# Performance work log

Measured on AMD Instinct MI355X. Metric: run time of the kernel, lower is better.

The kernel has to match this reference:

```python
import jax, jax.numpy as jnp
import numpy as np
from jax import lax

WINDOW = 11
C1 = (0.01 * 1) ** 2
C2 = (0.03 * 1) ** 2


def setup_inputs() -> dict:
    key = jax.random.key(0)
    kx, ky = jax.random.split(key)
    x = jax.random.uniform(kx, (8, 3, 512, 512), dtype=jnp.float32)
    y = jax.random.uniform(ky, (8, 3, 512, 512), dtype=jnp.float32)
    return {"x": x, "y": y}


def _window_sum(a):
    # sum over every overlapping WINDOW x WINDOW patch (stride 1, valid)
    return lax.reduce_window(a, 0.0, lax.add,
                             (1, 1, WINDOW, WINDOW),
                             (1, 1, 1, 1), 'VALID')


def reference(x, y):
    # x, y: [B, C, H, W] images in [0, 1]
    n = float(WINDOW * WINDOW)
    sx = _window_sum(x)
    sy = _window_sum(y)
    sxx = _window_sum(x * x)
    syy = _window_sum(y * y)
    sxy = _window_sum(x * y)
    mx = sx / n
    my = sy / n
    # unbiased variance / covariance (matches torch var(unbiased=True) and
    # the bessel-corrected covariance in the original)
    vx = (sxx - n * mx * mx) / (n - 1.0)
    vy = (syy - n * my * my) / (n - 1.0)
    cov = (sxy - n * mx * my) / (n - 1.0)
    ssim = (2.0 * mx * my + C1) * (2.0 * cov + C2) / (
        (mx * mx + my * my + C1) * (vx + vy + C2))
    # original averages over windows (dim 0) and channels (dim 2) -> per-batch
    return (1.0 - ssim.mean(axis=(1, 2, 3))) / 2.0
```

## Files before the change

kernel.cpp:

```cpp
#include <hip/hip_runtime.h>

#define WINDOW 11
#define H 512
#define W 512
#define OH 502
#define OW 502
#define NCH 3
#define BATCH 8
#define RSTRIPE 8
#define NSTRIPES 63
#define NGRP 5
#define GRPW 118
#define WAVES_PER_IMG (NSTRIPES * NGRP)
#define NWAVES (BATCH * NCH * WAVES_PER_IMG)
#define WAVES_PER_BATCH (NCH * WAVES_PER_IMG)
#define NXCD 8
#define CHUNK (NWAVES / NXCD)

#define NPIX_PER_BATCH (3.0f * 502.0f * 502.0f)

template <int CTRL, int RM>
__device__ __forceinline__ float scan_step(float x) {
    int s = __builtin_amdgcn_update_dpp(0, __builtin_bit_cast(int, x),
                                        CTRL, RM, 0xf, false);
    return x + __builtin_bit_cast(float, s);
}
__device__ __forceinline__ float wave_iscan(float x) {
    x = scan_step<0x111, 0xf>(x);
    x = scan_step<0x112, 0xf>(x);
    x = scan_step<0x114, 0xf>(x);
    x = scan_step<0x118, 0xf>(x);
    x = scan_step<0x142, 0xa>(x);
    x = scan_step<0x143, 0xc>(x);
    return x;
}

__device__ __forceinline__ float ssim_from(float sx, float sy, float s2, float sxy) {
    const float n = 121.0f;
    const float inv_n = 1.0f / 121.0f;
    const float inv_nm1 = 1.0f / 120.0f;
    const float c1 = 1e-4f;
    const float c2 = 9e-4f;
    float mx  = sx * inv_n;
    float my  = sy * inv_n;
    float mxy = mx * my;
    float m2  = mx * mx + my * my;
    float cov = (sxy - n * mxy) * inv_nm1;
    float v2  = (s2  - n * m2)  * inv_nm1;
    float num = (2.f * mxy + c1) * (2.f * cov + c2);
    float den = (m2 + c1) * (v2 + c2);
    return num * __builtin_amdgcn_rcpf(den);
}

__global__ __launch_bounds__(64) void ssim_main(const float* __restrict__ x,
                                                const float* __restrict__ y,
                                                float* __restrict__ partials) {
    const int lane = threadIdx.x & 63;

    const int wg    = blockIdx.x;
    const int w_lin = (wg % NXCD) * CHUNK + wg / NXCD;

    const int img = w_lin / WAVES_PER_IMG;
    const int rem = w_lin % WAVES_PER_IMG;
    const int grp = rem / NSTRIPES;
    const int rs  = rem % NSTRIPES;

    const int i0 = rs * RSTRIPE;
    const int i1 = min(i0 + RSTRIPE, OH);
    const int cstart = grp * GRPW;
    const int outw   = min(GRPW, OW - cstart);
    const int c0 = min(cstart + 2 * lane, W - 2);
    const bool tapActive = (2 * lane < outw);

    const float* __restrict__ xc = x + (size_t)img * H * W + c0;
    const float* __restrict__ yc = y + (size_t)img * H * W + c0;

    float4 v0 = make_float4(0.f, 0.f, 0.f, 0.f);
    float4 v1 = make_float4(0.f, 0.f, 0.f, 0.f);
#pragma unroll
    for (int r = 0; r < WINDOW; ++r) {
        float2 a = *(const float2*)(xc + (size_t)(i0 + r) * W);
        float2 b = *(const float2*)(yc + (size_t)(i0 + r) * W);
        v0.x += a.x; v0.y += b.x; v0.z += a.x * a.x + b.x * b.x; v0.w += a.x * b.x;
        v1.x += a.y; v1.y += b.y; v1.z += a.y * a.y + b.y * b.y; v1.w += a.y * b.y;
    }

#define LD(j, xo, yo, xn, yn) do {                                  \
        int jc_ = min((j), H - 1);                                   \
        int rn_ = min((j) + WINDOW, H - 1);                          \
        xo = *(const float2*)(xc + (size_t)jc_ * W);                 \
        yo = *(const float2*)(yc + (size_t)jc_ * W);                 \
        xn = *(const float2*)(xc + (size_t)rn_ * W);                 \
        yn = *(const float2*)(yc + (size_t)rn_ * W);                 \
    } while (0)

#define SLIDE(xo, yo, xn, yn) do {                                   \
        v0.x += xn.x - xo.x;                                          \
        v0.y += yn.x - yo.x;                                          \
        v0.z += xn.x * xn.x + yn.x * yn.x - xo.x * xo.x - yo.x * yo.x;\
        v0.w += xn.x * yn.x - xo.x * yo.x;                            \
        v1.x += xn.y - xo.y;                                          \
        v1.y += yn.y - yo.y;                                          \
        v1.z += xn.y * xn.y + yn.y * yn.y - xo.y * xo.y - yo.y * yo.y;\
        v1.w += xn.y * yn.y - xo.y * yo.y;                            \
    } while (0)

    float acc = 0.f;

#define COMPUTE() do {                                                        \
        float Tx = v0.x + v1.x, Ty = v0.y + v1.y;                             \
        float Tz = v0.z + v1.z, Tw = v0.w + v1.w;                             \
        float Sx = wave_iscan(Tx), Sy = wave_iscan(Ty);                       \
        float Sz = wave_iscan(Tz), Sw = wave_iscan(Tw);                       \
        int src = lane + 5;                                                   \
        float Ax = __shfl(Sx, src, 64), Ay = __shfl(Sy, src, 64);             \
        float Az = __shfl(Sz, src, 64), Aw = __shfl(Sw, src, 64);             \
        float Bx = __shfl(v1.x, src, 64), By = __shfl(v1.y, src, 64);         \
        float Bz = __shfl(v1.z, src, 64), Bw = __shfl(v1.w, src, 64);         \
        if (tapActive) {                                                      \
            acc += ssim_from(Ax - Bx - Sx + Tx, Ay - By - Sy + Ty,            \
                             Az - Bz - Sz + Tz, Aw - Bw - Sw + Tw);           \
            acc += ssim_from(Ax - Sx + v1.x, Ay - Sy + v1.y,                  \
                             Az - Sz + v1.z, Aw - Sw + v1.w);                 \
        }                                                                     \
    } while (0)

    float2 xoA, yoA, xnA, ynA, xoB, yoB, xnB, ynB;
    LD(i0,     xoA, yoA, xnA, ynA);
    LD(i0 + 1, xoB, yoB, xnB, ynB);
    for (int i = i0; i < i1; i += 2) {
        COMPUTE();
        SLIDE(xoA, yoA, xnA, ynA);
        LD(i + 2, xoA, yoA, xnA, ynA);
        COMPUTE();
        SLIDE(xoB, yoB, xnB, ynB);
        LD(i + 3, xoB, yoB, xnB, ynB);
    }

    for (int off = 32; off > 0; off >>= 1)
        acc += __shfl_down(acc, off, 64);
    if (lane == 0) partials[w_lin] = acc;
}

__global__ __launch_bounds__(256) void ssim_reduce(const float* __restrict__ partials,
                                                   float* __restrict__ out) {
    const int b = blockIdx.x;
    const int t = threadIdx.x;
    float s = 0.f;
    for (int k = t; k < WAVES_PER_BATCH; k += 256)
        s += partials[b * WAVES_PER_BATCH + k];
    for (int off = 32; off > 0; off >>= 1)
        s += __shfl_down(s, off, 64);
    __shared__ float red[4];
    int wid = t >> 6, lane = t & 63;
    if (lane == 0) red[wid] = s;
    __syncthreads();
    if (t == 0) {
        float tot = (red[0] + red[1]) + (red[2] + red[3]);
        out[b] = (1.0f - tot / NPIX_PER_BATCH) * 0.5f;
    }
}

extern "C" void kernel_launch(void* const* d_in, const int* in_sizes, int n_in,
                              void* d_out, int out_size, void* d_ws, size_t ws_size,
                              hipStream_t stream) {
    const float* x = (const float*)d_in[0];
    const float* y = (const float*)d_in[1];
    float* out      = (float*)d_out;
    float* partials = (float*)d_ws;

    ssim_main<<<NWAVES, 64, 0, stream>>>(x, y, partials);
    ssim_reduce<<<BATCH, 256, 0, stream>>>(partials, out);
}
```

Baseline: 28.29 us.

## Keep sliding-window rows in register ring and use taller row stripes

Stores the 11 rows of the current vertical window in a register ring buffer so each input row is loaded from memory once instead of twice (as new and as leaving row). Row stripes grow from 8 to 33 rows to amortize the 11-row prologue, with a mask for rows past the output edge. The reduce kernel drops its loop since partials per batch now fit one block. This trades fewer waves and higher register pressure for less memory traffic.

```diff
diff --git a/kernel.cpp b/kernel.cpp
--- a/kernel.cpp
+++ b/kernel.cpp
@@ -7,8 +7,8 @@
 #define OW 502
 #define NCH 3
 #define BATCH 8
-#define RSTRIPE 8
-#define NSTRIPES 63
+#define RSTRIPE 33
+#define NSTRIPES 16
 #define NGRP 5
 #define GRPW 118
 #define WAVES_PER_IMG (NSTRIPES * NGRP)
@@ -75,39 +75,42 @@
     const float* __restrict__ xc = x + (size_t)img * H * W + c0;
     const float* __restrict__ yc = y + (size_t)img * H * W + c0;
 
+    float2 fx[11], fy[11];
     float4 v0 = make_float4(0.f, 0.f, 0.f, 0.f);
     float4 v1 = make_float4(0.f, 0.f, 0.f, 0.f);
 #pragma unroll
     for (int r = 0; r < WINDOW; ++r) {
         float2 a = *(const float2*)(xc + (size_t)(i0 + r) * W);
         float2 b = *(const float2*)(yc + (size_t)(i0 + r) * W);
+        fx[r] = a; fy[r] = b;
         v0.x += a.x; v0.y += b.x; v0.z += a.x * a.x + b.x * b.x; v0.w += a.x * b.x;
         v1.x += a.y; v1.y += b.y; v1.z += a.y * a.y + b.y * b.y; v1.w += a.y * b.y;
     }
 
-#define LD(j, xo, yo, xn, yn) do {                                  \
+    float2 nx, ny;
+#define LDNEW(j) do {                                                \
         int jc_ = min((j), H - 1);                                   \
-        int rn_ = min((j) + WINDOW, H - 1);                          \
-        xo = *(const float2*)(xc + (size_t)jc_ * W);                 \
-        yo = *(const float2*)(yc + (size_t)jc_ * W);                 \
-        xn = *(const float2*)(xc + (size_t)rn_ * W);                 \
-        yn = *(const float2*)(yc + (size_t)rn_ * W);                 \
+        nx = *(const float2*)(xc + (size_t)jc_ * W);                 \
+        ny = *(const float2*)(yc + (size_t)jc_ * W);                 \
     } while (0)
 
-#define SLIDE(xo, yo, xn, yn) do {                                   \
-        v0.x += xn.x - xo.x;                                          \
-        v0.y += yn.x - yo.x;                                          \
-        v0.z += xn.x * xn.x + yn.x * yn.x - xo.x * xo.x - yo.x * yo.x;\
-        v0.w += xn.x * yn.x - xo.x * yo.x;                            \
-        v1.x += xn.y - xo.y;                                          \
-        v1.y += yn.y - yo.y;                                          \
-        v1.z += xn.y * xn.y + yn.y * yn.y - xo.y * xo.y - yo.y * yo.y;\
-        v1.w += xn.y * yn.y - xo.y * yo.y;                            \
+#define SLIDE(u) do {                                                 \
+        v0.x += nx.x - fx[u].x;                                       \
+        v0.y += ny.x - fy[u].x;                                       \
+        v0.z += nx.x * nx.x + ny.x * ny.x                             \
+              - fx[u].x * fx[u].x - fy[u].x * fy[u].x;                \
+        v0.w += nx.x * ny.x - fx[u].x * fy[u].x;                      \
+        v1.x += nx.y - fx[u].y;                                       \
+        v1.y += ny.y - fy[u].y;                                       \
+        v1.z += nx.y * nx.y + ny.y * ny.y                             \
+              - fx[u].y * fx[u].y - fy[u].y * fy[u].y;                \
+        v1.w += nx.y * ny.y - fx[u].y * fy[u].y;                      \
+        fx[u] = nx; fy[u] = ny;                                       \
     } while (0)
 
     float acc = 0.f;
 
-#define COMPUTE() do {                                                        \
+#define COMPUTE(rowActive) do {                                               \
         float Tx = v0.x + v1.x, Ty = v0.y + v1.y;                             \
         float Tz = v0.z + v1.z, Tw = v0.w + v1.w;                             \
         float Sx = wave_iscan(Tx), Sy = wave_iscan(Ty);                       \
@@ -117,7 +120,7 @@
         float Az = __shfl(Sz, src, 64), Aw = __shfl(Sw, src, 64);             \
         float Bx = __shfl(v1.x, src, 64), By = __shfl(v1.y, src, 64);         \
         float Bz = __shfl(v1.z, src, 64), Bw = __shfl(v1.w, src, 64);         \
-        if (tapActive) {                                                      \
+        if (tapActive & (rowActive)) {                                        \
             acc += ssim_from(Ax - Bx - Sx + Tx, Ay - By - Sy + Ty,            \
                              Az - Bz - Sz + Tz, Aw - Bw - Sw + Tw);           \
             acc += ssim_from(Ax - Sx + v1.x, Ay - Sy + v1.y,                  \
@@ -125,16 +128,15 @@
         }                                                                     \
     } while (0)
 
-    float2 xoA, yoA, xnA, ynA, xoB, yoB, xnB, ynB;
-    LD(i0,     xoA, yoA, xnA, ynA);
-    LD(i0 + 1, xoB, yoB, xnB, ynB);
-    for (int i = i0; i < i1; i += 2) {
-        COMPUTE();
-        SLIDE(xoA, yoA, xnA, ynA);
-        LD(i + 2, xoA, yoA, xnA, ynA);
-        COMPUTE();
-        SLIDE(xoB, yoB, xnB, ynB);
-        LD(i + 3, xoB, yoB, xnB, ynB);
+    LDNEW(i0 + WINDOW);
+    for (int base = i0; base < i1; base += 11) {
+#pragma unroll
+        for (int u = 0; u < 11; ++u) {
+            const int i = base + u;
+            COMPUTE(i < i1);
+            SLIDE(u);
+            LDNEW(i + WINDOW + 1);
+        }
     }
 
     for (int off = 32; off > 0; off >>= 1)
@@ -147,8 +149,8 @@
     const int b = blockIdx.x;
     const int t = threadIdx.x;
     float s = 0.f;
-    for (int k = t; k < WAVES_PER_BATCH; k += 256)
-        s += partials[b * WAVES_PER_BATCH + k];
+    if (t < WAVES_PER_BATCH)
+        s = partials[b * WAVES_PER_BATCH + t];
     for (int off = 32; off > 0; off >>= 1)
         s += __shfl_down(s, off, 64);
     __shared__ float red[4];
```

Result: faster. 26.89 us (-4.9%).
